# Kernel tuning notes

Hardware: AMD Instinct MI355X
Metric: run time of the kernel (lower is better)

## Reference

```python
import jax, jax.numpy as jnp
import numpy as np

D_MODEL = 1024
N_HEADS = 16
D_K = D_MODEL // N_HEADS
D_FF = 4096
LN_EPS = 1e-5


def _layer_norm(x, gamma, beta):
    mu = jnp.mean(x, axis=-1, keepdims=True)
    var = jnp.mean(jnp.square(x - mu), axis=-1, keepdims=True)
    return (x - mu) * jax.lax.rsqrt(var + LN_EPS) * gamma + beta


def setup_inputs() -> dict:
    key = jax.random.key(0)
    ks = jax.random.split(key, 16)
    B, S = 2, 2048
    x = jax.random.normal(ks[0], (B, S, D_MODEL), dtype=jnp.float32)
    # causal mask: True = masked (as used by masked_fill)
    mask = ~jnp.tril(jnp.ones((S, S), dtype=bool))
    s = 1.0 / np.sqrt(D_MODEL)
    sf = 1.0 / np.sqrt(D_FF)
    inp = {
        "x": x,
        "mask": mask,
        "ln1_g": jnp.ones((D_MODEL,), jnp.float32),
        "ln1_b": jnp.zeros((D_MODEL,), jnp.float32),
        "ln2_g": jnp.ones((D_MODEL,), jnp.float32),
        "ln2_b": jnp.zeros((D_MODEL,), jnp.float32),
        "Wq": jax.random.normal(ks[1], (D_MODEL, D_MODEL), jnp.float32) * s,
        "bq": jax.random.normal(ks[2], (D_MODEL,), jnp.float32) * s,
        "Wk": jax.random.normal(ks[3], (D_MODEL, D_MODEL), jnp.float32) * s,
        "bk": jax.random.normal(ks[4], (D_MODEL,), jnp.float32) * s,
        "Wv": jax.random.normal(ks[5], (D_MODEL, D_MODEL), jnp.float32) * s,
        "bv": jax.random.normal(ks[6], (D_MODEL,), jnp.float32) * s,
        "Wo": jax.random.normal(ks[7], (D_MODEL, D_MODEL), jnp.float32) * s,
        "bo": jax.random.normal(ks[8], (D_MODEL,), jnp.float32) * s,
        "W1": jax.random.normal(ks[9], (D_MODEL, D_FF), jnp.float32) * s,
        "b1": jax.random.normal(ks[10], (D_FF,), jnp.float32) * s,
        "W2": jax.random.normal(ks[11], (D_FF, D_MODEL), jnp.float32) * sf,
        "b2": jax.random.normal(ks[12], (D_MODEL,), jnp.float32) * sf,
    }
    return inp


def reference(x, mask, ln1_g, ln1_b, ln2_g, ln2_b,
              Wq, bq, Wk, bk, Wv, bv, Wo, bo, W1, b1, W2, b2):
    B, S, _ = x.shape
    normed = _layer_norm(x, ln1_g, ln1_b)
    # project and split heads: [B, H, S, Dk]
    def split_heads(t):
        return t.reshape(B, S, N_HEADS, D_K).transpose(0, 2, 1, 3)
    Q = split_heads(normed @ Wq + bq)
    K = split_heads(normed @ Wk + bk)
    V = split_heads(normed @ Wv + bv)
    qk = jnp.einsum("bhsd,bhtd->bhst", Q, K)  # [B, H, S, S]
    qk = jnp.where(mask, -jnp.inf, qk)  # mask applied BEFORE scaling, as in source
    attn = jax.nn.softmax(qk / np.sqrt(D_K), axis=-1)
    attn_out = jnp.einsum("bhst,bhtd->bhsd", attn, V)
    attn_out = attn_out.transpose(0, 2, 1, 3).reshape(B, S, D_MODEL)
    attn_out = attn_out @ Wo + bo
    res = attn_out + x  # dropout_p=0 (eval)
    h = _layer_norm(res, ln2_g, ln2_b)
    h = jax.nn.gelu(h @ W1 + b1, approximate=False)
    h = h @ W2 + b2
    return res + h
```

## Files before the change

### kernel.cpp

```cpp
#include <hip/hip_runtime.h>


typedef __bf16 bf16;
typedef __bf16 bf16x8 __attribute__((ext_vector_type(8)));
typedef float f32x4 __attribute__((ext_vector_type(4)));

#define NROWS 4096
#define DM 1024
#define SEQ 2048
#define NHEAD 16
#define DKH 64
#define DFF 4096
#define QSCALE 0.18033688f

#define GLL16(gptr, lptr) \
  __builtin_amdgcn_global_load_lds((const __attribute__((address_space(1))) void*)(gptr), \
                                   (__attribute__((address_space(3))) void*)(lptr), 16, 0, 0)

static char* g_scratch = nullptr;
namespace {
struct ScratchInit {
  ScratchInit() {
    void* p = nullptr;
    if (hipMalloc(&p, (size_t)128 * 1024 * 1024) == hipSuccess) g_scratch = (char*)p;
  }
};
static ScratchInit g_scratch_init;
}

__global__ __launch_bounds__(256) void ln_kernel(const float* __restrict__ inp,
                                                 const float* __restrict__ gamma,
                                                 const float* __restrict__ beta,
                                                 bf16* __restrict__ out) {
  int row = blockIdx.x;
  int t = threadIdx.x;
  float4 xv = *((const float4*)(inp + (size_t)row * DM) + t);
  float v[4] = {xv.x, xv.y, xv.z, xv.w};
  float s = 0.f, sq = 0.f;
#pragma unroll
  for (int i = 0; i < 4; i++) { s += v[i]; sq += v[i] * v[i]; }
#pragma unroll
  for (int m = 32; m >= 1; m >>= 1) { s += __shfl_xor(s, m); sq += __shfl_xor(sq, m); }
  __shared__ float rs[4], rq[4];
  int w = t >> 6, lane = t & 63;
  if (lane == 0) { rs[w] = s; rq[w] = sq; }
  __syncthreads();
  s = rs[0] + rs[1] + rs[2] + rs[3];
  sq = rq[0] + rq[1] + rq[2] + rq[3];
  float mu = s * (1.f / DM);
  float var = sq * (1.f / DM) - mu * mu;
  float rinv = rsqrtf(var + 1e-5f);
  float4 gv = *((const float4*)gamma + t);
  float4 bv = *((const float4*)beta + t);
  float g[4] = {gv.x, gv.y, gv.z, gv.w}, b[4] = {bv.x, bv.y, bv.z, bv.w};
  bf16 ov[4];
#pragma unroll
  for (int i = 0; i < 4; i++) ov[i] = (bf16)((v[i] - mu) * rinv * g[i] + b[i]);
  *(uint2*)(out + (size_t)row * DM + t * 4) = *(uint2*)ov;
}

__global__ __launch_bounds__(256) void concat_bias(const float* __restrict__ bq,
                                                   const float* __restrict__ bk,
                                                   const float* __restrict__ bv,
                                                   float* __restrict__ cat) {
  int i = blockIdx.x * 256 + threadIdx.x;
  float v = (i < 1024) ? bq[i] : (i < 2048 ? bk[i - 1024] : bv[i - 2048]);
  cat[i] = v;
}

__global__ __launch_bounds__(1024) void transpose_f32_bf16(const float* __restrict__ in,
                                                           bf16* __restrict__ out,
                                                           int R, int C) {
  __shared__ bf16 tile[32][33];
  int x = blockIdx.x * 32 + threadIdx.x;
  int y = blockIdx.y * 32 + threadIdx.y;
  tile[threadIdx.y][threadIdx.x] = (bf16)in[(size_t)y * C + x];
  __syncthreads();
  int ox = blockIdx.y * 32 + threadIdx.x;
  int oy = blockIdx.x * 32 + threadIdx.y;
  out[(size_t)oy * R + ox] = tile[threadIdx.x][threadIdx.y];
}

__global__ __launch_bounds__(1024) void transpose_bf16(const bf16* __restrict__ in,
                                                       bf16* __restrict__ out,
                                                       int R, int C) {
  __shared__ bf16 tile[32][33];
  size_t zoff = (size_t)blockIdx.z * (size_t)R * (size_t)C;
  int x = blockIdx.x * 32 + threadIdx.x;
  int y = blockIdx.y * 32 + threadIdx.y;
  tile[threadIdx.y][threadIdx.x] = in[zoff + (size_t)y * C + x];
  __syncthreads();
  int ox = blockIdx.y * 32 + threadIdx.x;
  int oy = blockIdx.x * 32 + threadIdx.y;
  out[zoff + (size_t)oy * R + ox] = tile[threadIdx.x][threadIdx.y];
}

#define BM 128
#define BK 64

#define EPI_QKV3 0
#define EPI_ATTN_RES 1
#define EPI_GELU 2
#define EPI_FFN2 3

template<int EPI, int BNT>
__global__ __launch_bounds__(256, 2) void gemm_bt(
    const bf16* __restrict__ A, const bf16* __restrict__ Bt,
    const float* __restrict__ bias, int Kd, int N,
    bf16* __restrict__ outb, float* __restrict__ outf,
    const float* __restrict__ add) {
  constexpr int MS = (BNT == 128) ? 4 : 2;
  __shared__ bf16 As[BM * BK];
  __shared__ bf16 Bs[BNT * BK];
  int t = threadIdx.x;
  int m0 = blockIdx.y * BM, n0 = blockIdx.x * BNT;
  int w = t >> 6, lane = t & 63, ln = lane & 15, quad = lane >> 4;
  int wm = (BNT == 128) ? (w >> 1) * 64 : w * 32;
  int wn = (BNT == 128) ? (w & 1) * 64 : 0;
  f32x4 acc[MS][4];
#pragma unroll
  for (int i = 0; i < MS; i++)
#pragma unroll
    for (int j = 0; j < 4; j++) acc[i][j] = (f32x4){0.f, 0.f, 0.f, 0.f};

  int lr = (t >> 3) & 7, lc = t & 7;
  int gcol = ((lc ^ lr) * 8);
  const bf16* Ab = A + (size_t)(m0 + w * 8 + lr) * Kd + gcol;
  const bf16* Bb = Bt + (size_t)(n0 + w * 8 + lr) * Kd + gcol;
  bf16* AsW = As + (w * 8) * BK;
  bf16* BsW = Bs + (w * 8) * BK;

  for (int k0 = 0; k0 < Kd; k0 += BK) {
    __syncthreads();
#pragma unroll
    for (int j = 0; j < 4; j++)
      GLL16(Ab + (size_t)(32 * j) * Kd + k0, AsW + 32 * j * BK);
#pragma unroll
    for (int j = 0; j < BNT / 32; j++)
      GLL16(Bb + (size_t)(32 * j) * Kd + k0, BsW + 32 * j * BK);
    __syncthreads();
#pragma unroll
    for (int kk = 0; kk < 2; kk++) {
      bf16x8 af[MS], bfr[4];
#pragma unroll
      for (int ms = 0; ms < MS; ms++) {
        int r = wm + ms * 16 + ln;
        af[ms] = *(const bf16x8*)(As + r * BK + (((kk * 4 + quad) ^ (r & 7)) * 8));
      }
#pragma unroll
      for (int ns = 0; ns < 4; ns++) {
        int r = wn + ns * 16 + ln;
        bfr[ns] = *(const bf16x8*)(Bs + r * BK + (((kk * 4 + quad) ^ (r & 7)) * 8));
      }
#pragma unroll
      for (int ms = 0; ms < MS; ms++)
#pragma unroll
        for (int ns = 0; ns < 4; ns++)
          acc[ms][ns] = __builtin_amdgcn_mfma_f32_16x16x32_bf16(af[ms], bfr[ns], acc[ms][ns], 0, 0, 0);
    }
  }

#pragma unroll
  for (int ms = 0; ms < MS; ms++) {
#pragma unroll
    for (int ns = 0; ns < 4; ns++) {
      int col = n0 + wn + ns * 16 + ln;
      float bv = bias[col];
#pragma unroll
      for (int r = 0; r < 4; r++) {
        int row = m0 + wm + ms * 16 + quad * 4 + r;
        float val = acc[ms][ns][r] + bv;
        if (EPI == EPI_QKV3) {
          int which = col >> 10, cc = col & 1023;
          int h = cc >> 6, dk = cc & 63;
          float sc = (which == 0) ? QSCALE : 1.f;
          int b = row >> 11, sx = row & 2047;
          outb[(size_t)which * (4 << 20) +
               ((((size_t)b * NHEAD + h) * SEQ) + sx) * DKH + dk] = (bf16)(val * sc);
        } else if (EPI == EPI_ATTN_RES) {
          size_t idx = (size_t)row * DM + col;
          outf[idx] = val + add[idx];
        } else if (EPI == EPI_GELU) {
          float gl = 0.5f * val * (1.f + erff(val * 0.7071067811865475f));
          outb[(size_t)row * N + col] = (bf16)gl;
        } else {
          size_t idx = (size_t)row * DM + col;
          outf[idx] = val + add[idx];
        }
      }
    }
  }
}

#define LSTR 72
#define OSTR 68

__global__ __launch_bounds__(256) void attn_kernel(
    const bf16* __restrict__ Q, const bf16* __restrict__ K,
    const bf16* __restrict__ Vt, bf16* __restrict__ out) {
  __shared__ float smem[4608];
  int lin = blockIdx.x;
  int bh = lin & 31;
  int qq = 63 - (lin >> 5);
  int t = threadIdx.x, w = t >> 6, lane = t & 63, ln = lane & 15, quad = lane >> 4;
  int qbase = qq * 32;
  size_t bhS = (size_t)bh * SEQ;
  const bf16* Vg0 = Vt + (size_t)bh * DKH * SEQ;
  bf16* Pw = (bf16*)smem + w * 32 * LSTR;

  bf16x8 qa[2][2];
#pragma unroll
  for (int m = 0; m < 2; m++)
#pragma unroll
    for (int ks = 0; ks < 2; ks++)
      qa[m][ks] = *(const bf16x8*)(Q + (bhS + qbase + m * 16 + ln) * DKH + ks * 32 + quad * 8);

  bf16x8 ones;
#pragma unroll
  for (int i = 0; i < 8; i++) ones[i] = (bf16)1.0f;

  f32x4 o[2][4];
#pragma unroll
  for (int m = 0; m < 2; m++)
#pragma unroll
    for (int i = 0; i < 4; i++) o[m][i] = (f32x4){0.f, 0.f, 0.f, 0.f};
  f32x4 accl[2] = {(f32x4){0.f, 0.f, 0.f, 0.f}, (f32x4){0.f, 0.f, 0.f, 0.f}};

  int ktmax = qq >> 1;
  for (int kt = w; kt <= ktmax; kt += 4) {
    const bf16* Kg = K + (bhS + kt * 64) * DKH;
    bf16x8 kbf[8], vbf[8];
#pragma unroll
    for (int ns = 0; ns < 4; ns++)
#pragma unroll
      for (int ks = 0; ks < 2; ks++)
        kbf[ns * 2 + ks] = *(const bf16x8*)(Kg + (ns * 16 + ln) * DKH + ks * 32 + quad * 8);
#pragma unroll
    for (int ns = 0; ns < 4; ns++)
#pragma unroll
      for (int ks = 0; ks < 2; ks++)
        vbf[ns * 2 + ks] = *(const bf16x8*)(Vg0 + (size_t)(ns * 16 + ln) * SEQ + kt * 64 + ks * 32 + quad * 8);

    f32x4 s[2][4];
#pragma unroll
    for (int m = 0; m < 2; m++)
#pragma unroll
      for (int ns = 0; ns < 4; ns++) s[m][ns] = (f32x4){0.f, 0.f, 0.f, 0.f};
#pragma unroll
    for (int ns = 0; ns < 4; ns++)
#pragma unroll
      for (int m = 0; m < 2; m++) {
        s[m][ns] = __builtin_amdgcn_mfma_f32_16x16x32_bf16(qa[m][0], kbf[ns * 2], s[m][ns], 0, 0, 0);
        s[m][ns] = __builtin_amdgcn_mfma_f32_16x16x32_bf16(qa[m][1], kbf[ns * 2 + 1], s[m][ns], 0, 0, 0);
      }
    if (kt == ktmax) {
#pragma unroll
      for (int m = 0; m < 2; m++)
#pragma unroll
        for (int ns = 0; ns < 4; ns++)
#pragma unroll
          for (int r = 0; r < 4; r++) {
            int qrow = qbase + m * 16 + quad * 4 + r;
            int kpos = kt * 64 + ns * 16 + ln;
            if (kpos > qrow) s[m][ns][r] = -30000.f;
          }
    }
#pragma unroll
    for (int m = 0; m < 2; m++)
#pragma unroll
      for (int ns = 0; ns < 4; ns++)
#pragma unroll
        for (int r = 0; r < 4; r++)
          Pw[(m * 16 + quad * 4 + r) * LSTR + ns * 16 + ln] =
              (bf16)__builtin_amdgcn_exp2f(s[m][ns][r]);
    bf16x8 pa[2][2];
#pragma unroll
    for (int m = 0; m < 2; m++) {
      pa[m][0] = *(const bf16x8*)(Pw + (m * 16 + ln) * LSTR + quad * 8);
      pa[m][1] = *(const bf16x8*)(Pw + (m * 16 + ln) * LSTR + 32 + quad * 8);
    }
#pragma unroll
    for (int m = 0; m < 2; m++) {
      accl[m] = __builtin_amdgcn_mfma_f32_16x16x32_bf16(pa[m][0], ones, accl[m], 0, 0, 0);
      accl[m] = __builtin_amdgcn_mfma_f32_16x16x32_bf16(pa[m][1], ones, accl[m], 0, 0, 0);
    }
#pragma unroll
    for (int ns2 = 0; ns2 < 4; ns2++)
#pragma unroll
      for (int m = 0; m < 2; m++) {
        o[m][ns2] = __builtin_amdgcn_mfma_f32_16x16x32_bf16(pa[m][0], vbf[ns2 * 2], o[m][ns2], 0, 0, 0);
        o[m][ns2] = __builtin_amdgcn_mfma_f32_16x16x32_bf16(pa[m][1], vbf[ns2 * 2 + 1], o[m][ns2], 0, 0, 0);
      }
  }

  float* Ob = smem;
  float* Lb = smem + 2 * 32 * OSTR;
  __syncthreads();
#pragma unroll
  for (int m = 0; m < 2; m++) {
    if (w < 2) {
#pragma unroll
      for (int ns2 = 0; ns2 < 4; ns2++)
#pragma unroll
        for (int r = 0; r < 4; r++)
          Ob[(w * 32 + m * 16 + quad * 4 + r) * OSTR + ns2 * 16 + ln] = o[m][ns2][r];
    }
    if (ln == 0) {
#pragma unroll
      for (int r = 0; r < 4; r++) Lb[w * 32 + m * 16 + quad * 4 + r] = accl[m][r];
    }
  }
  __syncthreads();
  if (w >= 2) {
#pragma unroll
    for (int m = 0; m < 2; m++)
#pragma unroll
      for (int ns2 = 0; ns2 < 4; ns2++)
#pragma unroll
        for (int r = 0; r < 4; r++) {
          int idx = ((w - 2) * 32 + m * 16 + quad * 4 + r) * OSTR + ns2 * 16 + ln;
          Ob[idx] += o[m][ns2][r];
        }
  }
  __syncthreads();

  int r = t >> 3, c0 = (t & 7) * 8;
  float l = Lb[r] + Lb[32 + r] + Lb[64 + r] + Lb[96 + r];
  float inv = 1.f / l;
  bf16 ov[8];
#pragma unroll
  for (int j = 0; j < 8; j++) {
    float v = Ob[r * OSTR + c0 + j] + Ob[(32 + r) * OSTR + c0 + j];
    ov[j] = (bf16)(v * inv);
  }
  int b = bh >> 4, h = bh & 15;
  *(uint4*)(out + ((size_t)b * SEQ + qbase + r) * DM + h * DKH + c0) = *(uint4*)ov;
}

extern "C" void kernel_launch(void* const* d_in, const int* in_sizes, int n_in,
                              void* d_out, int out_size, void* d_ws, size_t ws_size,
                              hipStream_t stream) {
  const float* x    = (const float*)d_in[0];
  const float* ln1g = (const float*)d_in[2];
  const float* ln1b = (const float*)d_in[3];
  const float* ln2g = (const float*)d_in[4];
  const float* ln2b = (const float*)d_in[5];
  const float* Wq = (const float*)d_in[6];   const float* bq = (const float*)d_in[7];
  const float* Wk = (const float*)d_in[8];   const float* bk = (const float*)d_in[9];
  const float* Wv = (const float*)d_in[10];  const float* bv = (const float*)d_in[11];
  const float* Wo = (const float*)d_in[12];  const float* bo = (const float*)d_in[13];
  const float* W1 = (const float*)d_in[14];  const float* b1 = (const float*)d_in[15];
  const float* W2 = (const float*)d_in[16];  const float* b2 = (const float*)d_in[17];
  float* outp = (float*)d_out;

  char* scratch = g_scratch ? g_scratch : (char*)d_ws;

  bf16* Wqt = (bf16*)scratch;
  bf16* Wkt = Wqt + (1 << 20);
  bf16* Wvt = Wkt + (1 << 20);
  bf16* Wot = Wvt + (1 << 20);
  bf16* W1t = Wot + (1 << 20);
  bf16* W2t = W1t + (4 << 20);
  bf16* normed = W2t + (4 << 20);
  bf16* Qb = normed + (4 << 20);
  bf16* Kb = Qb + (4 << 20);
  bf16* Vb = Kb + (4 << 20);
  bf16* Vtb = Vb + (4 << 20);
  bf16* attn_o = Vtb + (4 << 20);
  float* resf = (float*)(attn_o + (4 << 20));
  float* bias_cat = resf + (4 << 20);
  bf16* h1 = Qb;

  dim3 b256(256), b1k(32, 32);

  ln_kernel<<<NROWS, b256, 0, stream>>>(x, ln1g, ln1b, normed);
  concat_bias<<<12, b256, 0, stream>>>(bq, bk, bv, bias_cat);

  transpose_f32_bf16<<<dim3(32, 32), b1k, 0, stream>>>(Wq, Wqt, 1024, 1024);
  transpose_f32_bf16<<<dim3(32, 32), b1k, 0, stream>>>(Wk, Wkt, 1024, 1024);
  transpose_f32_bf16<<<dim3(32, 32), b1k, 0, stream>>>(Wv, Wvt, 1024, 1024);
  transpose_f32_bf16<<<dim3(32, 32), b1k, 0, stream>>>(Wo, Wot, 1024, 1024);
  transpose_f32_bf16<<<dim3(128, 32), b1k, 0, stream>>>(W1, W1t, 1024, 4096);
  transpose_f32_bf16<<<dim3(32, 128), b1k, 0, stream>>>(W2, W2t, 4096, 1024);

  gemm_bt<EPI_QKV3, 128><<<dim3(24, 32), b256, 0, stream>>>(
      normed, Wqt, bias_cat, 1024, 3072, Qb, nullptr, nullptr);

  transpose_bf16<<<dim3(2, 64, 32), b1k, 0, stream>>>(Vb, Vtb, 2048, 64);

  attn_kernel<<<dim3(2048), b256, 0, stream>>>(Qb, Kb, Vtb, attn_o);

  gemm_bt<EPI_ATTN_RES, 64><<<dim3(16, 32), b256, 0, stream>>>(
      attn_o, Wot, bo, 1024, 1024, nullptr, resf, x);

  ln_kernel<<<NROWS, b256, 0, stream>>>(resf, ln2g, ln2b, normed);

  gemm_bt<EPI_GELU, 128><<<dim3(32, 32), b256, 0, stream>>>(
      normed, W1t, b1, 1024, 4096, h1, nullptr, nullptr);

  gemm_bt<EPI_FFN2, 64><<<dim3(16, 32), b256, 0, stream>>>(
      h1, W2t, b2, 4096, 1024, nullptr, outp, resf);
}
```

Measured before the change: 403.0 us.

## Compute transposed S so P stays in registers for PV MFMA

Swaps the MFMA operand order so the score tile comes out transposed, which lets the exponentiated probabilities be packed to bf16 directly in registers with v_cvt_pk_bf16 and fed as the A operand of the PV MFMA. This removes the per-wave LDS round trip for P and shrinks shared memory. V loads are rearranged into two 8-byte halves to match the new k-index permutation, and the causal mask indices are swapped to follow. The cost is narrower, less coalesced V loads, and one __syncthreads before the reduction is dropped, which is only safe now that P no longer aliases the output buffer.

```diff
diff --git a/kernel.cpp b/kernel.cpp
--- a/kernel.cpp
+++ b/kernel.cpp
@@ -2,6 +2,7 @@
 
 
 typedef __bf16 bf16;
+typedef __bf16 bf16x4 __attribute__((ext_vector_type(4)));
 typedef __bf16 bf16x8 __attribute__((ext_vector_type(8)));
 typedef float f32x4 __attribute__((ext_vector_type(4)));
 
@@ -26,6 +27,12 @@
   }
 };
 static ScratchInit g_scratch_init;
+}
+
+__device__ inline unsigned cvt_pk_bf16(float lo, float hi) {
+  unsigned r;
+  asm("v_cvt_pk_bf16_f32 %0, %1, %2" : "=v"(r) : "v"(lo), "v"(hi));
+  return r;
 }
 
 __global__ __launch_bounds__(256) void ln_kernel(const float* __restrict__ inp,
@@ -192,13 +199,12 @@
   }
 }
 
-#define LSTR 72
 #define OSTR 68
 
 __global__ __launch_bounds__(256) void attn_kernel(
     const bf16* __restrict__ Q, const bf16* __restrict__ K,
     const bf16* __restrict__ Vt, bf16* __restrict__ out) {
-  __shared__ float smem[4608];
+  __shared__ float smem[2 * 32 * OSTR + 128];
   int lin = blockIdx.x;
   int bh = lin & 31;
   int qq = 63 - (lin >> 5);
@@ -206,7 +212,6 @@
   int qbase = qq * 32;
   size_t bhS = (size_t)bh * SEQ;
   const bf16* Vg0 = Vt + (size_t)bh * DKH * SEQ;
-  bf16* Pw = (bf16*)smem + w * 32 * LSTR;
 
   bf16x8 qa[2][2];
 #pragma unroll
@@ -238,8 +243,13 @@
 #pragma unroll
     for (int ns = 0; ns < 4; ns++)
 #pragma unroll
-      for (int ks = 0; ks < 2; ks++)
-        vbf[ns * 2 + ks] = *(const bf16x8*)(Vg0 + (size_t)(ns * 16 + ln) * SEQ + kt * 64 + ks * 32 + quad * 8);
+      for (int j = 0; j < 2; j++) {
+        const bf16* vrow = Vg0 + (size_t)(ns * 16 + ln) * SEQ + kt * 64 + j * 32 + quad * 4;
+        union { bf16x8 v; bf16x4 h[2]; } tmp;
+        tmp.h[0] = *(const bf16x4*)(vrow);
+        tmp.h[1] = *(const bf16x4*)(vrow + 16);
+        vbf[ns * 2 + j] = tmp.v;
+      }
 
     f32x4 s[2][4];
 #pragma unroll
@@ -250,8 +260,8 @@
     for (int ns = 0; ns < 4; ns++)
 #pragma unroll
       for (int m = 0; m < 2; m++) {
-        s[m][ns] = __builtin_amdgcn_mfma_f32_16x16x32_bf16(qa[m][0], kbf[ns * 2], s[m][ns], 0, 0, 0);
-        s[m][ns] = __builtin_amdgcn_mfma_f32_16x16x32_bf16(qa[m][1], kbf[ns * 2 + 1], s[m][ns], 0, 0, 0);
+        s[m][ns] = __builtin_amdgcn_mfma_f32_16x16x32_bf16(kbf[ns * 2], qa[m][0], s[m][ns], 0, 0, 0);
+        s[m][ns] = __builtin_amdgcn_mfma_f32_16x16x32_bf16(kbf[ns * 2 + 1], qa[m][1], s[m][ns], 0, 0, 0);
       }
     if (kt == ktmax) {
 #pragma unroll
@@ -260,8 +270,8 @@
         for (int ns = 0; ns < 4; ns++)
 #pragma unroll
           for (int r = 0; r < 4; r++) {
-            int qrow = qbase + m * 16 + quad * 4 + r;
-            int kpos = kt * 64 + ns * 16 + ln;
+            int qrow = qbase + m * 16 + ln;
+            int kpos = kt * 64 + ns * 16 + quad * 4 + r;
             if (kpos > qrow) s[m][ns][r] = -30000.f;
           }
     }
@@ -271,14 +281,19 @@
       for (int ns = 0; ns < 4; ns++)
 #pragma unroll
         for (int r = 0; r < 4; r++)
-          Pw[(m * 16 + quad * 4 + r) * LSTR + ns * 16 + ln] =
-              (bf16)__builtin_amdgcn_exp2f(s[m][ns][r]);
+          s[m][ns][r] = __builtin_amdgcn_exp2f(s[m][ns][r]);
     bf16x8 pa[2][2];
 #pragma unroll
-    for (int m = 0; m < 2; m++) {
-      pa[m][0] = *(const bf16x8*)(Pw + (m * 16 + ln) * LSTR + quad * 8);
-      pa[m][1] = *(const bf16x8*)(Pw + (m * 16 + ln) * LSTR + 32 + quad * 8);
-    }
+    for (int m = 0; m < 2; m++)
+#pragma unroll
+      for (int j = 0; j < 2; j++) {
+        union { bf16x8 v; unsigned u[4]; } pk;
+        pk.u[0] = cvt_pk_bf16(s[m][2 * j][0], s[m][2 * j][1]);
+        pk.u[1] = cvt_pk_bf16(s[m][2 * j][2], s[m][2 * j][3]);
+        pk.u[2] = cvt_pk_bf16(s[m][2 * j + 1][0], s[m][2 * j + 1][1]);
+        pk.u[3] = cvt_pk_bf16(s[m][2 * j + 1][2], s[m][2 * j + 1][3]);
+        pa[m][j] = pk.v;
+      }
 #pragma unroll
     for (int m = 0; m < 2; m++) {
       accl[m] = __builtin_amdgcn_mfma_f32_16x16x32_bf16(pa[m][0], ones, accl[m], 0, 0, 0);
@@ -295,7 +310,6 @@
 
   float* Ob = smem;
   float* Lb = smem + 2 * 32 * OSTR;
-  __syncthreads();
 #pragma unroll
   for (int m = 0; m < 2; m++) {
     if (w < 2) {
```

Measured after the change: 426.5 us. +5.8%, slower.
